# Optimization experiments

Measured on AMD Instinct MI355X. Metric: run time of the kernel, lower is better.

Reference implementation:

```python
import jax, jax.numpy as jnp
import numpy as np

PAD, BOS, EOS, UNK = 0, 1, 2, 3
B, S, V, D, L = 256, 512, 50000, 256, 128

def setup_inputs() -> dict:
    key = jax.random.key(0)
    ks = jax.random.split(key, 12)
    vocab_tensor = jax.random.randint(ks[0], (B, S), 4, V)
    parent_idx = jax.random.randint(ks[1], (B, S), 0, S)
    pbond = jax.random.randint(ks[2], (B, S), 0, 4)
    bond = jax.random.randint(ks[3], (B, S), 0, 4)
    patom = jax.random.randint(ks[4], (B, S), 0, 16)
    atom = jax.random.randint(ks[5], (B, S), 0, 16)
    btype = jax.random.randint(ks[6], (B, S), 0, 4)
    order_tensor = jnp.stack([parent_idx, pbond, bond, patom, atom, btype], axis=-1)
    lengths = jax.random.randint(ks[7], (B,), 1, S + 1)
    mask_tensor = jnp.arange(S)[None, :] < lengths[:, None]  # ragged prefix masks
    eps = jax.random.normal(ks[8], (B, L), dtype=jnp.float32)
    sc = 1.0 / np.sqrt(D)
    emb = jax.random.normal(ks[9], (V, D), dtype=jnp.float32) * sc
    Wm = jax.random.normal(ks[10], (D, L), dtype=jnp.float32) * sc
    Wv = jax.random.normal(ks[11], (D, L), dtype=jnp.float32) * sc
    Wlin = jax.random.normal(jax.random.fold_in(key, 20), (L, D), dtype=jnp.float32) / np.sqrt(L)
    Wout = jax.random.normal(jax.random.fold_in(key, 21), (D, D), dtype=jnp.float32) * sc
    return {
        'vocab_tensor': vocab_tensor, 'order_tensor': order_tensor, 'mask_tensor': mask_tensor,
        'eps': eps, 'emb': emb, 'Wm': Wm, 'bm': jnp.zeros((L,), jnp.float32),
        'Wv': Wv, 'bv': jnp.zeros((L,), jnp.float32), 'Wlin': Wlin,
        'blin': jnp.zeros((D,), jnp.float32), 'Wout': Wout, 'bout': jnp.zeros((D,), jnp.float32),
    }

def _forward(vocab_tensor, order_tensor, mask_tensor, eps, emb, Wm, bm, Wv, bv, Wlin, blin, Wout, bout):
    # --- mask bond-pos columns (torch.where assignments, vectorized) ---
    # (columns 1 and 2 set to -1 where masked; kept implicitly via vt/pad handling)
    # --- calc_chem_z path: masked vocab, parent gather, edge one-hot ---
    vt = jnp.where(mask_tensor, vocab_tensor, PAD)                      # [B,S]
    vocab_emb = emb[vt]                                                 # [B,S,D]
    oi = order_tensor[..., 0]
    oi = jnp.where(oi == -1, BOS, oi)
    parent = jnp.where(mask_tensor, jnp.take_along_axis(vt, oi, axis=1), PAD)
    parent = parent.at[:, 0].set(BOS)
    parent_emb = emb[parent]                                            # [B,S,D]
    idx = jnp.clip(order_tensor[..., 5] - 1, -1, None)
    edge_type = jnp.where((idx >= 0)[..., None],
                          jax.nn.one_hot(jnp.clip(idx, 0), 3, dtype=jnp.float32), 0.0)  # [B,S,3]
    # pooling stand-in for (undefined) StructureEncoder -> [B,D]
    m = mask_tensor[..., None].astype(jnp.float32)
    enc = ((vocab_emb + parent_emb) * m).sum(1) / jnp.maximum(m.sum(1), 1.0)
    enc = enc * (1.0 + 0.0 * edge_type.sum())  # keep edge_type in graph
    # --- LatentSampler ---
    mean = enc @ Wm + bm
    log_var = enc @ Wv + bv
    z = mean + eps * jnp.exp(0.5 * log_var)
    memory = z @ Wlin + blin                                            # [B,D]
    # --- vectorized bos/eos/pad sequence assembly (the hot loop in torch) ---
    inp = jnp.concatenate([jnp.full((B, 1), BOS, vocab_tensor.dtype), vocab_tensor], axis=1)  # [B,S+1]
    mask_ex = jnp.concatenate([jnp.ones((B, 1), bool), mask_tensor], axis=1)
    tgt = jnp.roll(inp, -1, axis=1)
    first_false = jnp.argmax(~mask_ex, axis=1)                          # first eos position
    has_false = jnp.any(~mask_ex, axis=1)
    pos = jnp.arange(S + 1)[None, :]
    tgt = jnp.where(has_false[:, None] & (pos == first_false[:, None] - 1), EOS, tgt)
    kill = has_false[:, None] & (pos >= first_false[:, None])
    tgt = jnp.where(kill, PAD, tgt)
    inp = jnp.where(kill, PAD, inp)
    # edge_index assembly (faithful, consumed by decoder in original)
    padneg = jnp.full((B, 1), -1, order_tensor.dtype)
    edge_index = jnp.concatenate([padneg, jnp.where(mask_tensor, order_tensor[..., 0], -2) + 1], axis=1)
    # --- embedding lookups + decoder stand-in + output head ---
    node_embed = emb[inp]                                               # [B,S+1,D]
    dec = node_embed + memory[:, None, :]
    dec = dec + 0.0 * edge_index[..., None].astype(jnp.float32)         # keep edge_index in graph
    word_emb = dec @ Wout + bout
    tgt_emb = emb[tgt]
    valid = (tgt != PAD)
    sq = (word_emb - tgt_emb) ** 2 * valid[..., None]
    token_loss = sq.sum() / jnp.maximum(valid.sum() * D, 1).astype(jnp.float32)
    kl = -0.5 * jnp.sum(1.0 + log_var - mean ** 2 - jnp.exp(log_var)) / B
    return token_loss, kl

def reference(vocab_tensor, order_tensor, mask_tensor, eps, emb, Wm, bm, Wv, bv, Wlin, blin, Wout, bout):
    return _forward(vocab_tensor, order_tensor, mask_tensor, eps, emb, Wm, bm, Wv, bv, Wlin, blin, Wout, bout)
```

## Files before the change

kernel.cpp:

```cpp
#include <hip/hip_runtime.h>

#define B_ 256
#define S_ 512
#define V_ 50000
#define D_ 256
#define L_ 128
#define PGRID 512

typedef __attribute__((ext_vector_type(8))) short short8;
typedef __attribute__((ext_vector_type(4))) float floatx4;

#define OFF_SQP  16
#define OFF_WT   (OFF_SQP + 256)
#define OFF_EB   (OFF_WT + 32768)
#define OFF_P    (OFF_EB + (V_ * D_ / 2))

__device__ __forceinline__ unsigned short f2bf(float x) {
    unsigned u = __float_as_uint(x);
    u += 0x7FFFu + ((u >> 16) & 1u);
    return (unsigned short)(u >> 16);
}
__device__ __forceinline__ unsigned pk2(float a, float b) {
    return (unsigned)f2bf(a) | ((unsigned)f2bf(b) << 16);
}
__device__ __forceinline__ float bf2f(unsigned short u) {
    return __uint_as_float(((unsigned)u) << 16);
}

__global__ __launch_bounds__(256) void wt_kernel(const float* __restrict__ Wout,
                                                 unsigned short* __restrict__ Wt,
                                                 float* __restrict__ ws) {
    __shared__ float sT[64][65];
    const int tid = threadIdx.x;
    if (blockIdx.x == 0) {
        if (tid < 16) ((int*)ws)[tid] = 0;
        ws[OFF_SQP + tid] = 0.f;
    }
    const int bx = blockIdx.x;
    const int k0 = (bx & 3) * 64, n0 = (bx >> 2) * 64;
    const int c = tid & 63, rg = tid >> 6;
#pragma unroll
    for (int i = 0; i < 16; ++i) {
        int r = rg * 16 + i;
        sT[c][r] = Wout[(k0 + r) * D_ + n0 + c];
    }
    __syncthreads();
#pragma unroll
    for (int i = 0; i < 16; ++i) {
        int r = rg * 16 + i;
        Wt[(size_t)(n0 + r) * D_ + k0 + c] = f2bf(sT[r][c]);
    }
}

__global__ __launch_bounds__(256, 2) void pgemm_kernel(
    const float* __restrict__ emb, const unsigned short* __restrict__ Wt,
    unsigned short* __restrict__ embb, unsigned short* __restrict__ P) {
    const int tid = threadIdx.x;
    const int wv = tid >> 6, lane = tid & 63;
    const int lo = lane & 15, hi = lane >> 4;
    const int NCH = V_ / 16;

    short8 bfr[4][8];
    const unsigned short* wbase = Wt + (size_t)(wv * 64 + lo) * D_ + hi * 8;
#pragma unroll
    for (int nt = 0; nt < 4; ++nt)
#pragma unroll
        for (int kk = 0; kk < 8; ++kk)
            bfr[nt][kk] = *(const short8*)(wbase + nt * 16 * D_ + kk * 32);

    for (int ch = blockIdx.x; ch < NCH; ch += PGRID) {
        const int row = ch * 16 + lo;
        const float* arow = emb + (size_t)row * D_ + hi * 8;
        short8 afr[8];
#pragma unroll
        for (int kk = 0; kk < 8; ++kk) {
            float4 f0 = *(const float4*)(arow + kk * 32);
            float4 f1 = *(const float4*)(arow + kk * 32 + 4);
            union { unsigned u[4]; short8 s; uint4 q; } cv;
            cv.u[0] = pk2(f0.x, f0.y);
            cv.u[1] = pk2(f0.z, f0.w);
            cv.u[2] = pk2(f1.x, f1.y);
            cv.u[3] = pk2(f1.z, f1.w);
            afr[kk] = cv.s;
            if (wv == 0)
                *(uint4*)(embb + (size_t)row * D_ + hi * 8 + kk * 32) = cv.q;
        }

        floatx4 acc[4];
#pragma unroll
        for (int nt = 0; nt < 4; ++nt) acc[nt] = (floatx4){0.f, 0.f, 0.f, 0.f};
#pragma unroll
        for (int kk = 0; kk < 8; ++kk)
#pragma unroll
            for (int nt = 0; nt < 4; ++nt)
                acc[nt] = __builtin_amdgcn_mfma_f32_16x16x32_bf16(
                    afr[kk], bfr[nt][kk], acc[nt], 0, 0, 0);

#pragma unroll
        for (int r = 0; r < 4; ++r) {
            unsigned short* prow = P + (size_t)(ch * 16 + hi * 4 + r) * D_ + wv * 64 + lo;
#pragma unroll
            for (int nt = 0; nt < 4; ++nt) prow[nt * 16] = f2bf(acc[nt][r]);
        }
    }
}

__global__ __launch_bounds__(1024) void enclat_kernel(
    const int* __restrict__ vocab, const int* __restrict__ order,
    const int* __restrict__ mask, const unsigned short* __restrict__ embb,
    const unsigned short* __restrict__ P, const float* __restrict__ eps,
    const float* __restrict__ Wm, const float* __restrict__ bm,
    const float* __restrict__ Wv, const float* __restrict__ bv,
    const float* __restrict__ Wlin, const float* __restrict__ blin,
    const float* __restrict__ Wout, const float* __restrict__ bout,
    float* __restrict__ ws, float* __restrict__ out) {
    __shared__ int s_id1[S_], s_id2[S_];
    __shared__ float4 s_part[15 * 64];
    __shared__ float s_enc[D_];
    __shared__ float s_mean[L_], s_lv[L_], s_z[L_], s_mem[D_], s_Q[D_];
    __shared__ float s_red[256];
    __shared__ float s_wred[16];
    __shared__ int s_cnt, s_prev;
    const int b = blockIdx.x;
    const int tid = threadIdx.x;
    float* kl_acc = ws + 1;
    int* vc_acc = (int*)ws + 2;
    int* done = (int*)ws + 3;
    float* sqp = ws + OFF_SQP;

    if (tid == 0) s_cnt = 0;
    __syncthreads();
    if (tid < S_) {
        int j = tid;
        int mk = mask[b * S_ + j];
        int id1 = 0, id2 = 0;
        if (mk) {
            id1 = vocab[b * S_ + j];
            if (j == 0) {
                id2 = 1;
            } else {
                int oi = order[(size_t)(b * S_ + j) * 6];
                if (oi == -1) oi = 1;
                id2 = mask[b * S_ + oi] ? vocab[b * S_ + oi] : 0;
            }
        }
        s_id1[j] = id1;
        s_id2[j] = id2;
        unsigned long long bal = __ballot(mk != 0);
        if ((tid & 63) == 0) atomicAdd(&s_cnt, __popcll(bal));
    }
    __syncthreads();
    const int cnt = s_cnt;
    const int jg = tid >> 6, d4 = tid & 63;
    const ushort4* eb4 = (const ushort4*)embb;
    float4 a = {0.f, 0.f, 0.f, 0.f};
#pragma unroll 4
    for (int j = jg; j < cnt; j += 16) {
        ushort4 x = eb4[(size_t)s_id1[j] * 64 + d4];
        ushort4 y = eb4[(size_t)s_id2[j] * 64 + d4];
        a.x += bf2f(x.x) + bf2f(y.x);
        a.y += bf2f(x.y) + bf2f(y.y);
        a.z += bf2f(x.z) + bf2f(y.z);
        a.w += bf2f(x.w) + bf2f(y.w);
    }
    if (jg) s_part[(jg - 1) * 64 + d4] = a;
    __syncthreads();
    if (jg == 0) {
#pragma unroll
        for (int g = 0; g < 15; ++g) {
            float4 p = s_part[g * 64 + d4];
            a.x += p.x; a.y += p.y; a.z += p.z; a.w += p.w;
        }
        float inv = 1.f / fmaxf((float)cnt, 1.f);
        a.x *= inv; a.y *= inv; a.z *= inv; a.w *= inv;
        ((float4*)s_enc)[d4] = a;
    }
    __syncthreads();
    float dot = 0.f;
    if (tid < 256) {
        const int l = tid & (L_ - 1);
        const float* W = (tid < L_) ? Wm : Wv;
        const float* bb = (tid < L_) ? bm : bv;
        dot = bb[l];
        for (int d = 0; d < D_; ++d) dot = fmaf(s_enc[d], W[d * L_ + l], dot);
        if (tid < L_) s_mean[l] = dot; else s_lv[l] = dot;
    }
    __syncthreads();
    float klp = 0.f;
    if (tid < L_) {
        float mn = s_mean[tid], lv = s_lv[tid];
        s_z[tid] = mn + eps[b * L_ + tid] * expf(0.5f * lv);
        klp = 1.f + lv - mn * mn - expf(lv);
    }
    if (tid < 256) s_red[tid] = klp;
    __syncthreads();
    for (int s = 128; s > 0; s >>= 1) {
        if (tid < s) s_red[tid] += s_red[tid + s];
        __syncthreads();
    }
    const float kl_part = s_red[0];
    if (tid < 256) {
        float mem = blin[tid];
        for (int l2 = 0; l2 < L_; ++l2) mem = fmaf(s_z[l2], Wlin[l2 * D_ + tid], mem);
        s_mem[tid] = mem;
    }
    __syncthreads();
    if (tid < 256) {
        float qv = bout[tid];
        for (int k = 0; k < D_; ++k) qv = fmaf(s_mem[k], Wout[k * D_ + tid], qv);
        s_Q[tid] = qv;
    }
    __syncthreads();
    const int lane = tid & 63;
    const int c = lane * 4;
    const float4 q4 = *(const float4*)(s_Q + c);
    float acc = 0.f;
    for (int j = jg; j <= cnt; j += 16) {
        const int inp = (j == 0) ? 1 : s_id1[j - 1];
        const int tgt = (j < cnt) ? s_id1[j] : ((cnt < S_) ? 2 : 1);
        const ushort4 pv = *(const ushort4*)(P + (size_t)inp * D_ + c);
        const ushort4 tv = *(const ushort4*)(embb + (size_t)tgt * D_ + c);
        float d0 = bf2f(pv.x) + q4.x - bf2f(tv.x);
        float d1 = bf2f(pv.y) + q4.y - bf2f(tv.y);
        float d2 = bf2f(pv.z) + q4.z - bf2f(tv.z);
        float d3 = bf2f(pv.w) + q4.w - bf2f(tv.w);
        acc += fmaf(d0, d0, fmaf(d1, d1, fmaf(d2, d2, d3 * d3)));
    }
#pragma unroll
    for (int off = 32; off; off >>= 1) acc += __shfl_down(acc, off, 64);
    if (lane == 0) s_wred[jg] = acc;
    __syncthreads();
    if (tid == 0) {
        float tot = 0.f;
#pragma unroll
        for (int g = 0; g < 16; ++g) tot += s_wred[g];
        sqp[b] = tot;
        atomicAdd(kl_acc, kl_part);
        atomicAdd(vc_acc, cnt + 1);
        __threadfence();
        s_prev = atomicAdd(done, 1);
    }
    __syncthreads();
    if (s_prev == B_ - 1) {
        float v = (tid < 256) ? atomicAdd(&sqp[tid], 0.f) : 0.f;
        if (tid < 256) s_red[tid] = v;
        __syncthreads();
        for (int s = 128; s > 0; s >>= 1) {
            if (tid < s) s_red[tid] += s_red[tid + s];
            __syncthreads();
        }
        if (tid == 0) {
            float kl = atomicAdd(kl_acc, 0.f);
            int vc = atomicAdd(vc_acc, 0);
            long long denom = (long long)vc * D_;
            if (denom < 1) denom = 1;
            out[0] = s_red[0] / (float)denom;
            out[1] = -0.5f * kl / (float)B_;
        }
    }
}

extern "C" void kernel_launch(void* const* d_in, const int* in_sizes, int n_in,
                              void* d_out, int out_size, void* d_ws, size_t ws_size,
                              hipStream_t stream) {
    const int* vocab = (const int*)d_in[0];
    const int* order = (const int*)d_in[1];
    const int* mask  = (const int*)d_in[2];
    const float* eps  = (const float*)d_in[3];
    const float* emb  = (const float*)d_in[4];
    const float* Wm   = (const float*)d_in[5];
    const float* bm   = (const float*)d_in[6];
    const float* Wv   = (const float*)d_in[7];
    const float* bv   = (const float*)d_in[8];
    const float* Wlin = (const float*)d_in[9];
    const float* blin = (const float*)d_in[10];
    const float* Wout = (const float*)d_in[11];
    const float* bout = (const float*)d_in[12];

    float* ws = (float*)d_ws;
    unsigned short* Wt = (unsigned short*)(ws + OFF_WT);
    unsigned short* embb = (unsigned short*)(ws + OFF_EB);
    unsigned short* P = (unsigned short*)(ws + OFF_P);

    wt_kernel<<<16, 256, 0, stream>>>(Wout, Wt, ws);
    pgemm_kernel<<<PGRID, 256, 0, stream>>>(emb, Wt, embb, P);
    enclat_kernel<<<B_, 1024, 0, stream>>>(vocab, order, mask, embb, P, eps,
                                           Wm, bm, Wv, bv, Wlin, blin, Wout, bout,
                                           ws, (float*)d_out);
}
```

Baseline: 194.8 us.

## Move emb bf16 conversion into prep kernel and prefetch A fragments in pgemm

Merges the Wout transpose with a grid-wide fp32-to-bf16 conversion of the embedding table into a single prep kernel. The GEMM kernel then reads the bf16 table directly and register-prefetches the next chunk's A operand while computing the current one. This is meant to remove the conversion and its redundant per-wave fp32 loads from the MFMA loop and to hide load latency. The cost is an extra full write and re-read of the bf16 table through memory, plus more registers in pgemm.

```diff
diff --git a/kernel.cpp b/kernel.cpp
--- a/kernel.cpp
+++ b/kernel.cpp
@@ -20,41 +20,49 @@
     u += 0x7FFFu + ((u >> 16) & 1u);
     return (unsigned short)(u >> 16);
 }
-__device__ __forceinline__ unsigned pk2(float a, float b) {
-    return (unsigned)f2bf(a) | ((unsigned)f2bf(b) << 16);
-}
 __device__ __forceinline__ float bf2f(unsigned short u) {
     return __uint_as_float(((unsigned)u) << 16);
 }
 
-__global__ __launch_bounds__(256) void wt_kernel(const float* __restrict__ Wout,
-                                                 unsigned short* __restrict__ Wt,
-                                                 float* __restrict__ ws) {
+__global__ __launch_bounds__(256) void prep_kernel(const float* __restrict__ emb,
+                                                   const float* __restrict__ Wout,
+                                                   unsigned short* __restrict__ embb,
+                                                   unsigned short* __restrict__ Wt,
+                                                   float* __restrict__ ws) {
     __shared__ float sT[64][65];
     const int tid = threadIdx.x;
     if (blockIdx.x == 0) {
         if (tid < 16) ((int*)ws)[tid] = 0;
         ws[OFF_SQP + tid] = 0.f;
     }
-    const int bx = blockIdx.x;
-    const int k0 = (bx & 3) * 64, n0 = (bx >> 2) * 64;
-    const int c = tid & 63, rg = tid >> 6;
-#pragma unroll
-    for (int i = 0; i < 16; ++i) {
-        int r = rg * 16 + i;
-        sT[c][r] = Wout[(k0 + r) * D_ + n0 + c];
-    }
-    __syncthreads();
-#pragma unroll
-    for (int i = 0; i < 16; ++i) {
-        int r = rg * 16 + i;
-        Wt[(size_t)(n0 + r) * D_ + k0 + c] = f2bf(sT[r][c]);
+    if (blockIdx.x < 16) {
+        const int bx = blockIdx.x;
+        const int k0 = (bx & 3) * 64, n0 = (bx >> 2) * 64;
+        const int c = tid & 63, rg = tid >> 6;
+#pragma unroll
+        for (int i = 0; i < 16; ++i) {
+            int r = rg * 16 + i;
+            sT[c][r] = Wout[(k0 + r) * D_ + n0 + c];
+        }
+        __syncthreads();
+#pragma unroll
+        for (int i = 0; i < 16; ++i) {
+            int r = rg * 16 + i;
+            Wt[(size_t)(n0 + r) * D_ + k0 + c] = f2bf(sT[r][c]);
+        }
+    }
+    const int N4 = V_ * D_ / 4;
+    for (int i = blockIdx.x * 256 + tid; i < N4; i += gridDim.x * 256) {
+        float4 v = ((const float4*)emb)[i];
+        ushort4 h;
+        h.x = f2bf(v.x); h.y = f2bf(v.y); h.z = f2bf(v.z); h.w = f2bf(v.w);
+        ((ushort4*)embb)[i] = h;
     }
 }
 
 __global__ __launch_bounds__(256, 2) void pgemm_kernel(
-    const float* __restrict__ emb, const unsigned short* __restrict__ Wt,
-    unsigned short* __restrict__ embb, unsigned short* __restrict__ P) {
+    const unsigned short* __restrict__ embb, const unsigned short* __restrict__ Wt,
+    unsigned short* __restrict__ P) {
     const int tid = threadIdx.x;
     const int wv = tid >> 6, lane = tid & 63;
     const int lo = lane & 15, hi = lane >> 4;
@@ -68,23 +76,18 @@
         for (int kk = 0; kk < 8; ++kk)
             bfr[nt][kk] = *(const short8*)(wbase + nt * 16 * D_ + kk * 32);
 
-    for (int ch = blockIdx.x; ch < NCH; ch += PGRID) {
-        const int row = ch * 16 + lo;
-        const float* arow = emb + (size_t)row * D_ + hi * 8;
-        short8 afr[8];
-#pragma unroll
-        for (int kk = 0; kk < 8; ++kk) {
-            float4 f0 = *(const float4*)(arow + kk * 32);
-            float4 f1 = *(const float4*)(arow + kk * 32 + 4);
-            union { unsigned u[4]; short8 s; uint4 q; } cv;
-            cv.u[0] = pk2(f0.x, f0.y);
-            cv.u[1] = pk2(f0.z, f0.w);
-            cv.u[2] = pk2(f1.x, f1.y);
-            cv.u[3] = pk2(f1.z, f1.w);
-            afr[kk] = cv.s;
-            if (wv == 0)
-                *(uint4*)(embb + (size_t)row * D_ + hi * 8 + kk * 32) = cv.q;
-        }
+    int ch = blockIdx.x;
+    const unsigned short* abase = embb + (size_t)(ch * 16 + lo) * D_ + hi * 8;
+    short8 acur[8];
+#pragma unroll
+    for (int kk = 0; kk < 8; ++kk) acur[kk] = *(const short8*)(abase + kk * 32);
+
+    for (; ch < NCH; ch += PGRID) {
+        const int chn = (ch + PGRID < NCH) ? (ch + PGRID) : ch;
+        const unsigned short* anext = embb + (size_t)(chn * 16 + lo) * D_ + hi * 8;
+        short8 anxt[8];
+#pragma unroll
+        for (int kk = 0; kk < 8; ++kk) anxt[kk] = *(const short8*)(anext + kk * 32);
 
         floatx4 acc[4];
 #pragma unroll
@@ -94,7 +97,7 @@
 #pragma unroll
             for (int nt = 0; nt < 4; ++nt)
                 acc[nt] = __builtin_amdgcn_mfma_f32_16x16x32_bf16(
-                    afr[kk], bfr[nt][kk], acc[nt], 0, 0, 0);
+                    acur[kk], bfr[nt][kk], acc[nt], 0, 0, 0);
 
 #pragma unroll
         for (int r = 0; r < 4; ++r) {
@@ -102,6 +105,8 @@
 #pragma unroll
             for (int nt = 0; nt < 4; ++nt) prow[nt * 16] = f2bf(acc[nt][r]);
         }
+#pragma unroll
+        for (int kk = 0; kk < 8; ++kk) acur[kk] = anxt[kk];
     }
 }
 
@@ -282,8 +287,8 @@
     unsigned short* embb = (unsigned short*)(ws + OFF_EB);
     unsigned short* P = (unsigned short*)(ws + OFF_P);
 
-    wt_kernel<<<16, 256, 0, stream>>>(Wout, Wt, ws);
-    pgemm_kernel<<<PGRID, 256, 0, stream>>>(emb, Wt, embb, P);
+    prep_kernel<<<2048, 256, 0, stream>>>(emb, Wout, embb, Wt, ws);
+    pgemm_kernel<<<PGRID, 256, 0, stream>>>(embb, Wt, P);
     enclat_kernel<<<B_, 1024, 0, stream>>>(vocab, order, mask, embb, P, eps,
                                            Wm, bm, Wv, bv, Wlin, blin, Wout, bout,
                                            ws, (float*)d_out);
```

Result: faster. 179.1 us (-8.0%).
